# Optimization experiments

Hardware: AMD Instinct MI355X
Metric: run time of the kernel (lower is better)

## Reference

```python
import jax, jax.numpy as jnp
import numpy as np

B, C, H, W = 4, 512, 64, 64
CQ = C // 8


def setup_inputs() -> dict:
    key = jax.random.key(0)
    ks = jax.random.split(key, 8)
    s = 0.05
    return {
        "x": jax.random.normal(ks[0], (B, C, H, W), dtype=jnp.float32),
        "wq": jax.random.normal(ks[1], (CQ, C), dtype=jnp.float32) * s,
        "bq": jax.random.normal(ks[2], (CQ,), dtype=jnp.float32) * s,
        "wk": jax.random.normal(ks[3], (CQ, C), dtype=jnp.float32) * s,
        "bk": jax.random.normal(ks[4], (CQ,), dtype=jnp.float32) * s,
        "wv": jax.random.normal(ks[5], (C, C), dtype=jnp.float32) * s,
        "bv": jax.random.normal(ks[6], (C,), dtype=jnp.float32) * s,
        "gamma": jax.random.normal(ks[7], (1,), dtype=jnp.float32) * 0.1,
    }


def reference(x, wq, bq, wk, bk, wv, bv, gamma):
    b, c, h, w = x.shape
    f = x.reshape(b, c, h * w)                       # [B, C, N]
    # 1x1 Conv1d == per-position matmul + bias
    q = jnp.einsum("dc,bcn->bdn", wq, f) + bq[:, None]   # [B, C/8, N]
    k = jnp.einsum("dc,bcn->bdn", wk, f) + bk[:, None]   # [B, C/8, N]
    v = jnp.einsum("dc,bcn->bdn", wv, f) + bv[:, None]   # [B, C, N]
    # query_key[b, i, j] = q_i . k_j  ; softmax over axis=1 (query index)
    qk = jnp.einsum("bdi,bdj->bij", q, k)                # [B, N, N]
    attn = jax.nn.softmax(qk, axis=1)
    o = jnp.einsum("bci,bij->bcj", v, attn)              # [B, C, N]
    return gamma * o.reshape(b, c, h, w) + x
```

## Files before the change

### kernel.cpp

```cpp
#include <hip/hip_runtime.h>
#include <hip/hip_bf16.h>

#define NB 4
#define NC 512
#define NN 4096
#define NM 640
#define IB 64
#define NT (NN / IB)
#define LOG2E 1.4426950408889634f

typedef __attribute__((ext_vector_type(8))) short bf16x8;
typedef __attribute__((ext_vector_type(4))) float f32x4;

__device__ __forceinline__ f32x4 mfma16(bf16x8 a, bf16x8 b, f32x4 c) {
  return __builtin_amdgcn_mfma_f32_16x16x32_bf16(a, b, c, 0, 0, 0);
}

__device__ __forceinline__ unsigned short f2bf(float f) {
  unsigned int u = __float_as_uint(f);
  u += 0x7fffu + ((u >> 16) & 1u);
  return (unsigned short)(u >> 16);
}

typedef const __attribute__((address_space(1))) char gchar_t;
typedef __attribute__((address_space(3))) char lchar_t;

__global__ void pack_w(const float* __restrict__ wq, const float* __restrict__ bq,
                       const float* __restrict__ wk, const float* __restrict__ bk,
                       const float* __restrict__ wv, const float* __restrict__ bv,
                       unsigned short* __restrict__ W, float* __restrict__ bias) {
  int idx = blockIdx.x * 256 + threadIdx.x;
  if (idx < NM * NC) {
    int r = idx >> 9, c = idx & (NC - 1);
    float v;
    if (r < 64) v = wq[r * NC + c];
    else if (r < 128) v = wk[(r - 64) * NC + c];
    else v = wv[(r - 128) * NC + c];
    W[idx] = f2bf(v);
  }
  if (idx < NM)
    bias[idx] = (idx < 64) ? bq[idx] : (idx < 128 ? bk[idx - 64] : bv[idx - 128]);
}

__global__ void xpose(const float* __restrict__ x, unsigned short* __restrict__ XT) {
  __shared__ float t[64][65];
  int b = blockIdx.z;
  int c0 = blockIdx.y * 64, n0 = blockIdx.x * 64;
  int tx = threadIdx.x & 63, ty = threadIdx.x >> 6;
  const float* xb = x + (size_t)b * NC * NN;
#pragma unroll
  for (int i = 0; i < 16; ++i) {
    int c = i * 4 + ty;
    t[c][tx] = xb[(size_t)(c0 + c) * NN + n0 + tx];
  }
  __syncthreads();
  unsigned short* xtb = XT + (size_t)b * NN * NC;
#pragma unroll
  for (int i = 0; i < 16; ++i) {
    int n = i * 4 + ty;
    xtb[(size_t)(n0 + n) * NC + c0 + tx] = f2bf(t[tx][n]);
  }
}

__global__ __launch_bounds__(512) void gemm_qkv(
    const unsigned short* __restrict__ W, const float* __restrict__ bias,
    const unsigned short* __restrict__ XT,
    unsigned short* __restrict__ QT, unsigned short* __restrict__ KT,
    unsigned short* __restrict__ V) {
  int b = blockIdx.z;
  int m0 = blockIdx.y * 80;
  int wave = threadIdx.x >> 6, lane = threadIdx.x & 63;
  int nw = blockIdx.x * 512 + wave * 64;
  int lcol = lane & 15, lkg = lane >> 4;
  const unsigned short* xtb = XT + (size_t)b * NN * NC;
  f32x4 acc[5][4] = {};
  for (int k0 = 0; k0 < NC; k0 += 32) {
    int ko = k0 + lkg * 8;
    bf16x8 afr[5], bfr[4];
#pragma unroll
    for (int i = 0; i < 5; ++i)
      afr[i] = *reinterpret_cast<const bf16x8*>(W + (size_t)(m0 + 16 * i + lcol) * NC + ko);
#pragma unroll
    for (int j = 0; j < 4; ++j)
      bfr[j] = *reinterpret_cast<const bf16x8*>(xtb + (size_t)(nw + 16 * j + lcol) * NC + ko);
#pragma unroll
    for (int i = 0; i < 5; ++i)
#pragma unroll
      for (int j = 0; j < 4; ++j)
        acc[i][j] = mfma16(afr[i], bfr[j], acc[i][j]);
  }
  int rbase = lkg * 4;
#pragma unroll
  for (int i = 0; i < 5; ++i) {
    int mrow = m0 + 16 * i;
    if (mrow < 128) {
      bool isq = mrow < 64;
      unsigned short* T = isq ? (QT + (size_t)b * NN * 64) : (KT + (size_t)b * NN * 64);
      int mb = mrow & 63;
      float sc = isq ? LOG2E : 1.0f;
#pragma unroll
      for (int j = 0; j < 4; ++j) {
        int n = nw + 16 * j + lcol;
        union { unsigned short h[4]; unsigned long long u; } pk;
#pragma unroll
        for (int r = 0; r < 4; ++r)
          pk.h[r] = f2bf((acc[i][j][r] + bias[mrow + rbase + r]) * sc);
        *reinterpret_cast<unsigned long long*>(T + (size_t)n * 64 + mb + rbase) = pk.u;
      }
    } else {
      unsigned short* vb = V + (size_t)b * NC * NN;
#pragma unroll
      for (int r = 0; r < 4; ++r) {
        int m = mrow + rbase + r;
        float bs = bias[m];
        int c = m - 128;
#pragma unroll
        for (int j = 0; j < 4; ++j) {
          int n = nw + 16 * j + lcol;
          vb[(size_t)c * NN + n] = f2bf(acc[i][j][r] + bs);
        }
      }
    }
  }
}

__global__ __launch_bounds__(512, 2) void attn_pv(
    const unsigned short* __restrict__ QT, const unsigned short* __restrict__ KT,
    const unsigned short* __restrict__ V, const float* __restrict__ x,
    const float* __restrict__ gamma, float* __restrict__ out) {
  int bid = blockIdx.x;
  int b = (bid & 7) >> 1;
  int jb = ((bid >> 3) << 1) | (bid & 1);
  int j0 = jb * 64;
  int wave = threadIdx.x >> 6, lane = threadIdx.x & 63;
  int lcol = lane & 15, lkg = lane >> 4;
  int sw = wave >> 1;
  int fnh = wave & 1;

  __shared__ __align__(16) unsigned short vlds[2][512 * IB];
  __shared__ __align__(16) unsigned short plds[2][64 * IB];
  __shared__ float sml[4][16][4];

  const unsigned short* qt = QT + (size_t)b * NN * 64;
  const unsigned short* kt = KT + (size_t)b * NN * 64;
  const unsigned short* vp = V + (size_t)b * NC * NN;

  const int lrow = lane >> 3;
  const int lswz = ((lane & 7) ^ lrow) << 3;
  lchar_t* vbase = (lchar_t*)vlds;

  auto stage = [&](int itv) {
    int i0 = (itv & (NT - 1)) * IB;
    lchar_t* lb = vbase + (size_t)(itv & 1) * (512 * IB * 2) + wave * (64 * IB * 2);
#pragma unroll
    for (int q = 0; q < 8; ++q) {
      const unsigned short* gp = vp + (size_t)(wave * 64 + q * 8 + lrow) * NN + i0 + lswz;
      __builtin_amdgcn_global_load_lds((gchar_t*)gp, lb + q * 1024, 16, 0, 0);
    }
  };

  bf16x8 kfr[2][2];
#pragma unroll
  for (int f = 0; f < 2; ++f) {
    int fn = 2 * fnh + f;
#pragma unroll
    for (int ks = 0; ks < 2; ++ks)
      kfr[f][ks] = *reinterpret_cast<const bf16x8*>(
          kt + (size_t)(j0 + 16 * fn + lcol) * 64 + ks * 32 + lkg * 8);
  }

  f32x4 oacc[4][4] = {};
  float l_loc[2] = {0.f, 0.f};

  stage(0);
  bf16x8 qA[2], qB[2];
  {
    int row = sw * 16 + lcol;
    qA[0] = *reinterpret_cast<const bf16x8*>(qt + (size_t)row * 64 + lkg * 8);
    qA[1] = *reinterpret_cast<const bf16x8*>(qt + (size_t)row * 64 + 32 + lkg * 8);
  }

#define PV_ITER(IT, QC, QN)                                                       \
  {                                                                               \
    const int it_ = (IT);                                                         \
    stage(it_ + 1);                                                               \
    f32x4 s[2] = {};                                                              \
    _Pragma("unroll") for (int ks = 0; ks < 2; ++ks)                              \
      _Pragma("unroll") for (int f = 0; f < 2; ++f)                               \
        s[f] = mfma16(QC[ks], kfr[f][ks], s[f]);                                  \
    {                                                                             \
      int row = ((it_ + 1) & (NT - 1)) * IB + sw * 16 + lcol;                     \
      QN[0] = *reinterpret_cast<const bf16x8*>(qt + (size_t)row * 64 + lkg * 8);  \
      QN[1] = *reinterpret_cast<const bf16x8*>(qt + (size_t)row * 64 + 32 + lkg * 8); \
    }                                                                             \
    char* pb = (char*)plds[it_ & 1];                                              \
    _Pragma("unroll") for (int f = 0; f < 2; ++f) {                               \
      int j = 16 * (2 * fnh + f) + lcol;                                          \
      float p0 = exp2f(s[f][0]), p1 = exp2f(s[f][1]);                             \
      float p2 = exp2f(s[f][2]), p3 = exp2f(s[f][3]);                             \
      l_loc[f] += (p0 + p1) + (p2 + p3);                                          \
      union { unsigned short h[4]; unsigned long long u; } pk;                    \
      pk.h[0] = f2bf(p0); pk.h[1] = f2bf(p1);                                     \
      pk.h[2] = f2bf(p2); pk.h[3] = f2bf(p3);                                     \
      int bo = (j * 128 + sw * 32 + lkg * 8) ^ ((j & 7) << 4);                    \
      *reinterpret_cast<unsigned long long*>(pb + bo) = pk.u;                     \
    }                                                                             \
    asm volatile("s_waitcnt vmcnt(10) lgkmcnt(0)" ::: "memory");                  \
    __builtin_amdgcn_s_barrier();                                                 \
    asm volatile("" ::: "memory");                                                \
    const char* vb = (const char*)vlds[it_ & 1];                                  \
    __builtin_amdgcn_s_setprio(1);                                                \
    _Pragma("unroll") for (int ks = 0; ks < 2; ++ks) {                            \
      bf16x8 pfr[4];                                                              \
      _Pragma("unroll") for (int fn = 0; fn < 4; ++fn) {                          \
        int j = 16 * fn + lcol;                                                   \
        int bo = (j * 128 + ks * 64 + lkg * 16) ^ ((j & 7) << 4);                 \
        pfr[fn] = *reinterpret_cast<const bf16x8*>(pb + bo);                      \
      }                                                                           \
      _Pragma("unroll") for (int cm = 0; cm < 4; ++cm) {                          \
        int cr = 64 * wave + 16 * cm + lcol;                                      \
        int u = (ks * 4 + lkg) ^ (cr & 7);                                        \
        bf16x8 vfr = *reinterpret_cast<const bf16x8*>(vb + cr * 128 + u * 16);    \
        _Pragma("unroll") for (int fn = 0; fn < 4; ++fn)                          \
          oacc[cm][fn] = mfma16(vfr, pfr[fn], oacc[cm][fn]);                      \
      }                                                                           \
    }                                                                             \
    __builtin_amdgcn_s_setprio(0);                                                \
  }

  for (int it2 = 0; it2 < NT; it2 += 2) {
    PV_ITER(it2 + 0, qA, qB);
    PV_ITER(it2 + 1, qB, qA);
  }
#undef PV_ITER

#pragma unroll
  for (int f = 0; f < 2; ++f) {
    l_loc[f] += __shfl_xor(l_loc[f], 16);
    l_loc[f] += __shfl_xor(l_loc[f], 32);
  }
  if (lane < 16) {
#pragma unroll
    for (int f = 0; f < 2; ++f) sml[2 * fnh + f][lane][sw] = l_loc[f];
  }
  __syncthreads();
  float lj[4];
#pragma unroll
  for (int fn = 0; fn < 4; ++fn) {
    const float* p = sml[fn][lcol];
    lj[fn] = (p[0] + p[1]) + (p[2] + p[3]);
  }

  float g = gamma[0];
  const float* xb = x + (size_t)b * NC * NN;
  float* ob = out + (size_t)b * NC * NN;
#pragma unroll
  for (int fn = 0; fn < 4; ++fn) {
    float sc = g / lj[fn];
    int j = j0 + 16 * fn + lcol;
#pragma unroll
    for (int cm = 0; cm < 4; ++cm) {
      int c = 64 * wave + 16 * cm + lkg * 4;
#pragma unroll
      for (int r = 0; r < 4; ++r) {
        size_t idx = (size_t)(c + r) * NN + j;
        ob[idx] = oacc[cm][fn][r] * sc + xb[idx];
      }
    }
  }
}

extern "C" void kernel_launch(void* const* d_in, const int* in_sizes, int n_in,
                              void* d_out, int out_size, void* d_ws, size_t ws_size,
                              hipStream_t stream) {
  const float* x  = (const float*)d_in[0];
  const float* wq = (const float*)d_in[1];
  const float* bq = (const float*)d_in[2];
  const float* wk = (const float*)d_in[3];
  const float* bk = (const float*)d_in[4];
  const float* wv = (const float*)d_in[5];
  const float* bv = (const float*)d_in[6];
  const float* gm = (const float*)d_in[7];
  float* out = (float*)d_out;

  char* ws = (char*)d_ws;
  unsigned short* XT = (unsigned short*)(ws);
  unsigned short* Vb = (unsigned short*)(ws + (size_t)16 * 1024 * 1024);
  unsigned short* QT = (unsigned short*)(ws + (size_t)32 * 1024 * 1024);
  unsigned short* KT = (unsigned short*)(ws + (size_t)34 * 1024 * 1024);
  unsigned short* Wp = (unsigned short*)(ws + (size_t)36 * 1024 * 1024);
  float* biasp = (float*)(ws + (size_t)36 * 1024 * 1024 + 704 * 1024);

  pack_w<<<(NM * NC + 255) / 256, 256, 0, stream>>>(wq, bq, wk, bk, wv, bv, Wp, biasp);
  xpose<<<dim3(NN / 64, NC / 64, NB), 256, 0, stream>>>(x, XT);
  gemm_qkv<<<dim3(NN / 512, NM / 80, NB), 512, 0, stream>>>(Wp, biasp, XT, QT, KT, Vb);
  attn_pv<<<256, 512, 0, stream>>>(QT, KT, Vb, x, gm, out);
}
```

Baseline: 154.2 us.

## Double attn_pv waves per block, halving channel rows and S tiles per wave

Launches attn_pv with 1024 threads (16 waves) instead of 512. Each wave now owns 32 output channels and one 16x16 score tile, instead of 64 channels and two tiles. V staging and the wait counts are adjusted to match. The aim is more waves per CU to hide memory and LDS latency, and fewer registers per wave, since LDS use caps the CU at one block. In exchange, every wave still reads the full P tile from LDS, so P reads double, and each barrier now synchronizes more waves.

```diff
diff --git a/kernel.cpp b/kernel.cpp
--- a/kernel.cpp
+++ b/kernel.cpp
@@ -124,7 +124,7 @@
   }
 }
 
-__global__ __launch_bounds__(512, 2) void attn_pv(
+__global__ __launch_bounds__(1024, 4) void attn_pv(
     const unsigned short* __restrict__ QT, const unsigned short* __restrict__ KT,
     const unsigned short* __restrict__ V, const float* __restrict__ x,
     const float* __restrict__ gamma, float* __restrict__ out) {
@@ -134,8 +134,8 @@
   int j0 = jb * 64;
   int wave = threadIdx.x >> 6, lane = threadIdx.x & 63;
   int lcol = lane & 15, lkg = lane >> 4;
-  int sw = wave >> 1;
-  int fnh = wave & 1;
+  int sw = wave & 3;
+  int fq = wave >> 2;
 
   __shared__ __align__(16) unsigned short vlds[2][512 * IB];
   __shared__ __align__(16) unsigned short plds[2][64 * IB];
@@ -151,26 +151,25 @@
 
   auto stage = [&](int itv) {
     int i0 = (itv & (NT - 1)) * IB;
-    lchar_t* lb = vbase + (size_t)(itv & 1) * (512 * IB * 2) + wave * (64 * IB * 2);
-#pragma unroll
-    for (int q = 0; q < 8; ++q) {
-      const unsigned short* gp = vp + (size_t)(wave * 64 + q * 8 + lrow) * NN + i0 + lswz;
+    lchar_t* lb = vbase + (size_t)(itv & 1) * (512 * IB * 2) + wave * (32 * IB * 2);
+#pragma unroll
+    for (int q = 0; q < 4; ++q) {
+      const unsigned short* gp = vp + (size_t)(wave * 32 + q * 8 + lrow) * NN + i0 + lswz;
       __builtin_amdgcn_global_load_lds((gchar_t*)gp, lb + q * 1024, 16, 0, 0);
     }
   };
 
-  bf16x8 kfr[2][2];
-#pragma unroll
-  for (int f = 0; f < 2; ++f) {
-    int fn = 2 * fnh + f;
-#pragma unroll
-    for (int ks = 0; ks < 2; ++ks)
-      kfr[f][ks] = *reinterpret_cast<const bf16x8*>(
-          kt + (size_t)(j0 + 16 * fn + lcol) * 64 + ks * 32 + lkg * 8);
-  }
-
-  f32x4 oacc[4][4] = {};
-  float l_loc[2] = {0.f, 0.f};
+  bf16x8 kfr[2];
+#pragma unroll
+  for (int ks = 0; ks < 2; ++ks)
+    kfr[ks] = *reinterpret_cast<const bf16x8*>(
+        kt + (size_t)(j0 + 16 * fq + lcol) * 64 + ks * 32 + lkg * 8);
+
+  f32x4 oacc[2][4] = {};
+  float l_loc = 0.f;
+
+  const int jw = 16 * fq + lcol;
+  const int pwoff = (jw * 128 + sw * 32 + lkg * 8) ^ ((jw & 7) << 4);
 
   stage(0);
   bf16x8 qA[2], qB[2];
@@ -184,28 +183,25 @@
   {                                                                               \
     const int it_ = (IT);                                                         \
     stage(it_ + 1);                                                               \
-    f32x4 s[2] = {};                                                              \
-    _Pragma("unroll") for (int ks = 0; ks < 2; ++ks)                              \
-      _Pragma("unroll") for (int f = 0; f < 2; ++f)                               \
-        s[f] = mfma16(QC[ks], kfr[f][ks], s[f]);                                  \
+    f32x4 s = {};                                                                 \
+    s = mfma16(QC[0], kfr[0], s);                                                 \
+    s = mfma16(QC[1], kfr[1], s);                                                 \
     {                                                                             \
       int row = ((it_ + 1) & (NT - 1)) * IB + sw * 16 + lcol;                     \
       QN[0] = *reinterpret_cast<const bf16x8*>(qt + (size_t)row * 64 + lkg * 8);  \
       QN[1] = *reinterpret_cast<const bf16x8*>(qt + (size_t)row * 64 + 32 + lkg * 8); \
     }                                                                             \
     char* pb = (char*)plds[it_ & 1];                                              \
-    _Pragma("unroll") for (int f = 0; f < 2; ++f) {                               \
-      int j = 16 * (2 * fnh + f) + lcol;                                          \
-      float p0 = exp2f(s[f][0]), p1 = exp2f(s[f][1]);                             \
-      float p2 = exp2f(s[f][2]), p3 = exp2f(s[f][3]);                             \
-      l_loc[f] += (p0 + p1) + (p2 + p3);                                          \
+    {                                                                             \
+      float p0 = exp2f(s[0]), p1 = exp2f(s[1]);                                   \
+      float p2 = exp2f(s[2]), p3 = exp2f(s[3]);                                   \
+      l_loc += (p0 + p1) + (p2 + p3);                                             \
       union { unsigned short h[4]; unsigned long long u; } pk;                    \
       pk.h[0] = f2bf(p0); pk.h[1] = f2bf(p1);                                     \
       pk.h[2] = f2bf(p2); pk.h[3] = f2bf(p3);                                     \
-      int bo = (j * 128 + sw * 32 + lkg * 8) ^ ((j & 7) << 4);                    \
-      *reinterpret_cast<unsigned long long*>(pb + bo) = pk.u;                     \
+      *reinterpret_cast<unsigned long long*>(pb + pwoff) = pk.u;                  \
     }                                                                             \
-    asm volatile("s_waitcnt vmcnt(10) lgkmcnt(0)" ::: "memory");                  \
+    asm volatile("s_waitcnt vmcnt(6) lgkmcnt(0)" ::: "memory");                   \
     __builtin_amdgcn_s_barrier();                                                 \
     asm volatile("" ::: "memory");                                                \
     const char* vb = (const char*)vlds[it_ & 1];                                  \
@@ -217,8 +213,8 @@
         int bo = (j * 128 + ks * 64 + lkg * 16) ^ ((j & 7) << 4);                 \
         pfr[fn] = *reinterpret_cast<const bf16x8*>(pb + bo);                      \
       }                                                                           \
-      _Pragma("unroll") for (int cm = 0; cm < 4; ++cm) {                          \
-        int cr = 64 * wave + 16 * cm + lcol;                                      \
+      _Pragma("unroll") for (int cm = 0; cm < 2; ++cm) {                          \
+        int cr = 32 * wave + 16 * cm + lcol;                                      \
         int u = (ks * 4 + lkg) ^ (cr & 7);                                        \
         bf16x8 vfr = *reinterpret_cast<const bf16x8*>(vb + cr * 128 + u * 16);    \
         _Pragma("unroll") for (int fn = 0; fn < 4; ++fn)                          \
@@ -234,15 +230,9 @@
   }
 #undef PV_ITER
 
-#pragma unroll
-  for (int f = 0; f < 2; ++f) {
-    l_loc[f] += __shfl_xor(l_loc[f], 16);
-    l_loc[f] += __shfl_xor(l_loc[f], 32);
-  }
-  if (lane < 16) {
-#pragma unroll
-    for (int f = 0; f < 2; ++f) sml[2 * fnh + f][lane][sw] = l_loc[f];
-  }
+  l_loc += __shfl_xor(l_loc, 16);
+  l_loc += __shfl_xor(l_loc, 32);
+  if (lane < 16) sml[fq][lane][sw] = l_loc;
   __syncthreads();
   float lj[4];
 #pragma unroll
@@ -259,8 +249,8 @@
     float sc = g / lj[fn];
     int j = j0 + 16 * fn + lcol;
 #pragma unroll
-    for (int cm = 0; cm < 4; ++cm) {
-      int c = 64 * wave + 16 * cm + lkg * 4;
+    for (int cm = 0; cm < 2; ++cm) {
+      int c = 32 * wave + 16 * cm + lkg * 4;
 #pragma unroll
       for (int r = 0; r < 4; ++r) {
         size_t idx = (size_t)(c + r) * NN + j;
@@ -294,5 +284,5 @@
   pack_w<<<(NM * NC + 255) / 256, 256, 0, stream>>>(wq, bq, wk, bk, wv, bv, Wp, biasp);
   xpose<<<dim3(NN / 64, NC / 64, NB), 256, 0, stream>>>(x, XT);
   gemm_qkv<<<dim3(NN / 512, NM / 80, NB), 512, 0, stream>>>(Wp, biasp, XT, QT, KT, Vb);
-  attn_pv<<<256, 512, 0, stream>>>(QT, KT, Vb, x, gm, out);
-}
+  attn_pv<<<256, 1024, 0, stream>>>(QT, KT, Vb, x, gm, out);
+}
```

Result: slower. 163.3 us (+5.9%).
